# Optimization experiments

Measured on AMD Instinct MI355X. Metric: run time of the kernel, lower is better.

The kernel has to match this reference:

```python
import jax, jax.numpy as jnp
import numpy as np

N = 50000   # nodes
F = 128     # v_feats
K = 128     # filters
H = 3       # multi_head
M = 10      # fixed neighbor count (hardcoded repeat(1,10,1) in source)


def setup_inputs() -> dict:
    key = jax.random.key(0)
    ks = jax.random.split(key, 10)
    vertices = jax.random.normal(ks[0], (N, F), jnp.float32)
    nh_indices = jax.random.randint(ks[1], (N, M), 0, N)
    int_indices = jax.random.randint(ks[2], (N, M), 0, N)
    nh_edges = jax.random.uniform(ks[3], (N, M), jnp.float32)
    int_edges = jax.random.uniform(ks[4], (N, M), jnp.float32)
    is_int = jax.random.randint(ks[5], (N,), 0, 2)
    scale = 0.05
    Wvc = jax.random.normal(ks[6], (H, F, K), jnp.float32) * scale
    Wvn_int = jax.random.normal(ks[7], (H, F, K), jnp.float32) * scale
    Wvn_nh = jax.random.normal(ks[8], (H, F, K), jnp.float32) * scale
    a = jax.random.normal(ks[9], (H, 2 * K, 1), jnp.float32) * scale
    bv = jnp.zeros((H, K), jnp.float32)
    return dict(vertices=vertices, nh_indices=nh_indices, int_indices=int_indices,
                nh_edges=nh_edges, int_edges=int_edges, is_int=is_int,
                Wvc=Wvc, bv=bv, Wvn_int=Wvn_int, Wvn_nh=Wvn_nh, a=a)


def reference(vertices, nh_indices, int_indices, nh_edges, int_edges, is_int,
              Wvc, bv, Wvn_int, Wvn_nh, a):
    n = vertices.shape[0]
    k = a.shape[1] // 2
    # Project center and neighbor features for all heads at once.
    Zc = jnp.einsum('nf,hfk->hnk', vertices, Wvc)        # [H,N,K]
    Vint = jnp.einsum('nf,hfk->hnk', vertices, Wvn_int)  # [H,N,K]
    Vnh = jnp.einsum('nf,hfk->hnk', vertices, Wvn_nh)    # [H,N,K]
    # cat((neighbor, center)) @ a  ==  neighbor @ a[:k] + center @ a[k:]
    a_n = a[:, :k, 0]  # [H,K]
    a_c = a[:, k:, 0]  # [H,K]
    e_center = jnp.einsum('hnk,hk->hn', Zc, a_c)[:, :, None]  # [H,N,1]

    def branch(Vside, idx, edges):
        mask = (idx != -1).astype(vertices.dtype)           # [N,M], -1 = pad
        g = Vside[:, idx]                                   # [H,N,M,K] gather
        e = jnp.einsum('hnmk,hk->hnm', g, a_n) + e_center   # [H,N,M]
        # faithful to source: scores zeroed (not -inf) by mask/edges before softmax
        e = e * mask[None] * edges[None]
        alpha = jax.nn.softmax(e, axis=2)                   # [H,N,M]
        norm = jnp.maximum(mask.sum(axis=1), 1.0)           # [N]
        Zn = jnp.einsum('hnmk,hnm->hnk', g * mask[None, :, :, None], alpha)
        return Zn / norm[None, :, None]

    Zn_inter = branch(Vint, int_indices, int_edges)
    Zn_chain = branch(Vnh, nh_indices, nh_edges)
    z = jax.nn.relu(Zc + Zn_inter + Zn_chain + bv[:, None, :])  # [H,N,K]
    # torch.cat(head outputs, dim=1) -> [N, H*K]
    return jnp.transpose(z, (1, 0, 2)).reshape(n, -1)
```

## Files before the change

### kernel.cpp

```cpp
#include <hip/hip_runtime.h>
#include <stdint.h>

#define N_V 50000
#define F_DIM 128
#define K_DIM 128
#define H_DIM 3
#define M_DIM 10
#define TILES_PER_BLK 4

using bf16x8 = __attribute__((ext_vector_type(8))) short;
using f32x4  = __attribute__((ext_vector_type(4))) float;
using f32x2  = __attribute__((ext_vector_type(2))) float;
using h4     = __attribute__((ext_vector_type(4))) _Float16;

__device__ inline unsigned short f2bf(float f) {
    union { float f; uint32_t u; } v; v.f = f;
    uint32_t u = v.u;
    u += 0x7fffu + ((u >> 16) & 1u);
    return (unsigned short)(u >> 16);
}

__device__ inline uint32_t pkh2(float a, float b) {
    union { _Float16 h[2]; uint32_t u; } v;
    v.h[0] = (_Float16)a; v.h[1] = (_Float16)b;
    return v.u;
}

#define LDS_AS __attribute__((address_space(3)))
__device__ inline void gl2lds16(const void* g, void* l) {
    __builtin_amdgcn_global_load_lds(
        (const __attribute__((address_space(1))) unsigned int*)g,
        (LDS_AS unsigned int*)l, 16, 0, 0);
}

#define WTOT (9 * 128 * 128)
#define XCH  (N_V * 16)
#define WACT (9 * 128)

__global__ void prep(const float* __restrict__ Wvc,
                     const float* __restrict__ Wvn_int,
                     const float* __restrict__ Wvn_nh,
                     const float* __restrict__ X,
                     const float* __restrict__ a,
                     unsigned short* __restrict__ Wt,
                     unsigned short* __restrict__ Xb,
                     unsigned short* __restrict__ wab) {
    int idx = blockIdx.x * 256 + threadIdx.x;
    if (idx < WTOT) {
        int b   = idx >> 14;
        int rem = idx & 16383;
        int k = rem >> 7;
        int f = rem & 127;
        int h = b / 3, t = b - 3 * h;
        const float* src = (t == 0) ? Wvc : (t == 1) ? Wvn_int : Wvn_nh;
        Wt[idx] = f2bf(src[(h * 128 + f) * 128 + k]);
        return;
    }
    int xi = idx - WTOT;
    if (xi < XCH) {
        const float4* Xv = (const float4*)X;
        float4 v0 = Xv[xi * 2];
        float4 v1 = Xv[xi * 2 + 1];
        uint4 o;
        o.x = (uint32_t)f2bf(v0.x) | ((uint32_t)f2bf(v0.y) << 16);
        o.y = (uint32_t)f2bf(v0.z) | ((uint32_t)f2bf(v0.w) << 16);
        o.z = (uint32_t)f2bf(v1.x) | ((uint32_t)f2bf(v1.y) << 16);
        o.w = (uint32_t)f2bf(v1.z) | ((uint32_t)f2bf(v1.w) << 16);
        *(uint4*)&Xb[(size_t)xi * 8] = o;
        return;
    }
    int wi = xi - XCH;
    if (wi < WACT) {
        int b = wi >> 7, f = wi & 127;
        int h = b / 3, t = b - 3 * h;
        const float* src = (t == 0) ? Wvc : (t == 1) ? Wvn_int : Wvn_nh;
        const float4* wrow = (const float4*)&src[(h * 128 + f) * 128];
        const float4* av   = (const float4*)&a[h * 256 + (t == 0 ? 128 : 0)];
        float acc = 0.f;
        #pragma unroll 8
        for (int c = 0; c < 32; ++c) {
            float4 w = wrow[c], x = av[c];
            acc += w.x * x.x + w.y * x.y + w.z * x.z + w.w * x.w;
        }
        wab[b * 128 + f] = f2bf(acc);
    }
}

__global__ __launch_bounds__(256, 3) void gemm_kernel(
    const unsigned short* __restrict__ Xb,
    const unsigned short* __restrict__ Wt,
    const unsigned short* __restrict__ wab,
    _Float16* __restrict__ zc16,
    uint8_t* __restrict__ Vint,
    uint8_t* __restrict__ Vnh,
    float* __restrict__ ec4,
    float* __restrict__ ei4,
    float* __restrict__ en4) {
    __shared__ unsigned short As[2][64 * 128];

    const int tid  = threadIdx.x;
    const int b    = blockIdx.y;
    const int hh   = b / 3;
    const int tt   = b - 3 * hh;
    const int wv   = tid >> 6;
    const int lane = tid & 63;
    const int q    = lane >> 4;
    const int ln   = lane & 15;
    const int cb   = (wv >> 1) * 64;
    const int rb   = (wv & 1) * 32;
    const int m0   = blockIdx.x * (64 * TILES_PER_BLK);

    auto stage = [&](int buf, int tile) {
        const int mb = m0 + tile * 64;
        #pragma unroll
        for (int it = 0; it < 4; ++it) {
            int c16 = it * 256 + tid;
            int r   = c16 >> 4;
            int p   = c16 & 15;
            int lch = p ^ (r & 15);
            int gr  = mb + r;
            if (gr >= N_V) gr = 0;
            gl2lds16(Xb + (size_t)gr * 128 + lch * 8, &As[buf][c16 * 8]);
        }
    };

    stage(0, 0);

    const unsigned short* Wb = Wt + (size_t)b * 16384;
    bf16x8 bfr[4][4];
    #pragma unroll
    for (int ct = 0; ct < 4; ++ct) {
        int col = cb + 4 * ln + ct;
        #pragma unroll
        for (int kk = 0; kk < 4; ++kk)
            bfr[ct][kk] = *(const bf16x8*)&Wb[col * 128 + kk * 32 + q * 8];
    }

    const bool do_e = (b == 0) && (wv < 2);
    bf16x8 wz[4];
    if (do_e) {
        #pragma unroll
        for (int kk = 0; kk < 4; ++kk) {
            bf16x8 z = {0, 0, 0, 0, 0, 0, 0, 0};
            if (ln < 9) z = *(const bf16x8*)&wab[ln * 128 + kk * 32 + q * 8];
            wz[kk] = z;
        }
    }

    __syncthreads();

    const int c0 = cb + 4 * ln;
    #pragma unroll
    for (int t = 0; t < TILES_PER_BLK; ++t) {
        const int mb = m0 + t * 64;

        if (t + 1 < TILES_PER_BLK) stage((t + 1) & 1, t + 1);

        f32x4 acc[2][4];
        #pragma unroll
        for (int rt = 0; rt < 2; ++rt)
            #pragma unroll
            for (int ct = 0; ct < 4; ++ct) acc[rt][ct] = (f32x4){0.f, 0.f, 0.f, 0.f};

        #pragma unroll
        for (int rt = 0; rt < 2; ++rt) {
            bf16x8 afr[4];
            const int r = rb + rt * 16 + ln;
            #pragma unroll
            for (int kk = 0; kk < 4; ++kk) {
                int p = (kk * 4 + q) ^ ln;
                afr[kk] = *(const bf16x8*)&As[t & 1][r * 128 + p * 8];
            }
            #pragma unroll
            for (int kk = 0; kk < 4; ++kk)
                #pragma unroll
                for (int ct = 0; ct < 4; ++ct)
                    acc[rt][ct] = __builtin_amdgcn_mfma_f32_16x16x32_bf16(
                        afr[kk], bfr[ct][kk], acc[rt][ct], 0, 0, 0);

            if (do_e) {
                f32x4 ae = (f32x4){0.f, 0.f, 0.f, 0.f};
                #pragma unroll
                for (int kk = 0; kk < 4; ++kk)
                    ae = __builtin_amdgcn_mfma_f32_16x16x32_bf16(
                        afr[kk], wz[kk], ae, 0, 0, 0);
                if (ln < 9) {
                    int h2 = ln / 3, t2 = ln - 3 * h2;
                    float* ep = (t2 == 0) ? ec4 : (t2 == 1) ? ei4 : en4;
                    #pragma unroll
                    for (int rg = 0; rg < 4; ++rg) {
                        int gr = mb + rb + rt * 16 + q * 4 + rg;
                        if (gr < N_V) ep[gr * 4 + h2] = ae[rg];
                    }
                }
            }
        }

        __syncthreads();

        if (tt == 0) {
            #pragma unroll
            for (int rt = 0; rt < 2; ++rt)
                #pragma unroll
                for (int rg = 0; rg < 4; ++rg) {
                    int gr = mb + rb + rt * 16 + q * 4 + rg;
                    if (gr >= N_V) continue;
                    uint2 s;
                    s.x = pkh2(acc[rt][0][rg], acc[rt][1][rg]);
                    s.y = pkh2(acc[rt][2][rg], acc[rt][3][rg]);
                    *(uint2*)&zc16[(size_t)gr * 384 + hh * 128 + c0] = s;
                }
        } else {
            uint8_t* Vside = (tt == 1) ? Vint : Vnh;
            #pragma unroll
            for (int rt = 0; rt < 2; ++rt)
                #pragma unroll
                for (int rg = 0; rg < 4; ++rg) {
                    int gr = mb + rb + rt * 16 + q * 4 + rg;
                    if (gr >= N_V) continue;
                    int pk = __builtin_amdgcn_cvt_pk_fp8_f32(
                        acc[rt][0][rg], acc[rt][1][rg], 0, false);
                    pk = __builtin_amdgcn_cvt_pk_fp8_f32(
                        acc[rt][2][rg], acc[rt][3][rg], pk, true);
                    *(uint32_t*)&Vside[((size_t)gr * 3 + hh) * 128 + c0] =
                        (uint32_t)pk;
                }
        }
    }
}

__global__ __launch_bounds__(512) void attn_kernel(
    const int* __restrict__ nh_idx, const int* __restrict__ int_idx,
    const float* __restrict__ nh_edge, const float* __restrict__ int_edge,
    const float* __restrict__ bv,
    const uint8_t* __restrict__ Vint,
    const uint8_t* __restrict__ Vnh,
    const float* __restrict__ ec4, const float* __restrict__ ei4,
    const float* __restrict__ en4,
    const _Float16* __restrict__ zc16,
    float* __restrict__ out, int n0) {
    const int wv   = threadIdx.x >> 6;
    const int lane = threadIdx.x & 63;
    const int n    = n0 + blockIdx.x * 8 + wv;
    if (n >= N_V) return;
    const int g  = lane >> 4;
    const int gl = lane & 15;

    const bool part = (g <= 1) && (gl < M_DIM);
    int jm = -1; float wm = 0.f;
    if (part) {
        const int*   idx = (g == 0) ? int_idx  : nh_idx;
        const float* ed  = (g == 0) ? int_edge : nh_edge;
        jm = idx[n * M_DIM + gl];
        wm = ed[n * M_DIM + gl];
    }
    const bool  valid = part && (jm >= 0);
    const int   jc    = valid ? jm : 0;
    const float vfl   = valid ? 1.f : 0.f;

    const int src_base = (g < 2 ? 0 : 16) + (g & 1) * 5;
    int jrow[5];
    #pragma unroll
    for (int i = 0; i < 5; ++i) jrow[i] = __shfl(jc, src_base + i, 64);

    const uint8_t* Vb = (g < 2) ? Vint : Vnh;
    uint2 pv[3][5];
    #pragma unroll
    for (int i = 0; i < 5; ++i) {
        const uint8_t* base = Vb + (size_t)jrow[i] * 384 + gl * 8;
        #pragma unroll
        for (int h = 0; h < H_DIM; ++h)
            pv[h][i] = *(const uint2*)(base + h * 128);
    }
    float4 ev = make_float4(0.f, 0.f, 0.f, 0.f);
    if (part) ev = *(const float4*)&(((g == 0) ? ei4 : en4)[jc * 4]);
    const float4 ecv = *(const float4*)&ec4[n * 4];

    float4 zc[3], bb[3];
    if (g < 2) {
        #pragma unroll
        for (int h = 0; h < H_DIM; ++h) {
            h4 z = *(const h4*)&zc16[(size_t)n * 384 + h * 128 + gl * 8 + g * 4];
            zc[h] = make_float4((float)z[0], (float)z[1], (float)z[2], (float)z[3]);
            bb[h] = *(const float4*)&bv[h * 128 + gl * 8 + g * 4];
        }
    }

    float cf = vfl;
    #pragma unroll
    for (int off = 1; off < 16; off <<= 1) cf += __shfl_xor(cf, off, 64);
    const float cnorm = fmaxf(cf, 1.f);

    #pragma unroll
    for (int h = 0; h < H_DIM; ++h) {
        const float eh  = (h == 0) ? ev.x  : (h == 1) ? ev.y  : ev.z;
        const float ech = (h == 0) ? ecv.x : (h == 1) ? ecv.y : ecv.z;

        float l = (part && valid) ? (eh + ech) * wm : 0.f;
        float ex = part ? __expf(l) : 0.f;
        float sv = ex;
        #pragma unroll
        for (int off = 1; off < 16; off <<= 1) sv += __shfl_xor(sv, off, 64);
        float alphap = valid ? ex / (sv * cnorm) : 0.f;

        f32x2 acc2[4];
        #pragma unroll
        for (int c = 0; c < 4; ++c) acc2[c] = (f32x2){0.f, 0.f};
        #pragma unroll
        for (int i = 0; i < 5; ++i) {
            float al = __shfl(alphap, src_base + i, 64);
            f32x2 al2 = (f32x2){al, al};
            uint2 p  = pv[h][i];
            f32x2 f01 = __builtin_amdgcn_cvt_pk_f32_fp8(p.x, false);
            f32x2 f23 = __builtin_amdgcn_cvt_pk_f32_fp8(p.x, true);
            f32x2 f45 = __builtin_amdgcn_cvt_pk_f32_fp8(p.y, false);
            f32x2 f67 = __builtin_amdgcn_cvt_pk_f32_fp8(p.y, true);
            acc2[0] += al2 * f01;
            acc2[1] += al2 * f23;
            acc2[2] += al2 * f45;
            acc2[3] += al2 * f67;
        }
        #pragma unroll
        for (int c = 0; c < 4; ++c) {
            f32x2 v = acc2[c];
            v.x += __shfl_xor(v.x, 16, 64);
            v.y += __shfl_xor(v.y, 16, 64);
            v.x += __shfl_xor(v.x, 32, 64);
            v.y += __shfl_xor(v.y, 32, 64);
            acc2[c] = v;
        }
        if (g < 2) {
            size_t o = (size_t)n * 384 + h * 128 + gl * 8 + g * 4;
            float4 zn;
            if (g == 0) zn = make_float4(acc2[0].x, acc2[0].y, acc2[1].x, acc2[1].y);
            else        zn = make_float4(acc2[2].x, acc2[2].y, acc2[3].x, acc2[3].y);
            float4 r;
            r.x = fmaxf(zc[h].x + zn.x + bb[h].x, 0.f);
            r.y = fmaxf(zc[h].y + zn.y + bb[h].y, 0.f);
            r.z = fmaxf(zc[h].z + zn.z + bb[h].z, 0.f);
            r.w = fmaxf(zc[h].w + zn.w + bb[h].w, 0.f);
            *(float4*)&out[o] = r;
        }
    }
}

extern "C" void kernel_launch(void* const* d_in, const int* in_sizes, int n_in,
                              void* d_out, int out_size, void* d_ws, size_t ws_size,
                              hipStream_t stream) {
    const float* vertices    = (const float*)d_in[0];
    const int*   nh_indices  = (const int*)d_in[1];
    const int*   int_indices = (const int*)d_in[2];
    const float* nh_edges    = (const float*)d_in[3];
    const float* int_edges   = (const float*)d_in[4];
    const float* Wvc     = (const float*)d_in[6];
    const float* bv      = (const float*)d_in[7];
    const float* Wvn_int = (const float*)d_in[8];
    const float* Wvn_nh  = (const float*)d_in[9];
    const float* a       = (const float*)d_in[10];
    float* out = (float*)d_out;

    char* ws = (char*)d_ws;
    size_t off = 0;
    unsigned short* Wt = (unsigned short*)(ws + off);
    off += (size_t)WTOT * 2;                  off = (off + 255) & ~(size_t)255;
    unsigned short* wab = (unsigned short*)(ws + off);
    off += (size_t)WACT * 2;                  off = (off + 255) & ~(size_t)255;
    unsigned short* Xb = (unsigned short*)(ws + off);
    off += (size_t)N_V * 128 * 2;             off = (off + 255) & ~(size_t)255;
    uint8_t* Vint = (uint8_t*)(ws + off);
    off += (size_t)H_DIM * N_V * 128;         off = (off + 255) & ~(size_t)255;
    uint8_t* Vnh = (uint8_t*)(ws + off);
    off += (size_t)H_DIM * N_V * 128;         off = (off + 255) & ~(size_t)255;
    _Float16* zc16 = (_Float16*)(ws + off);
    off += (size_t)N_V * 384 * 2;             off = (off + 255) & ~(size_t)255;
    float* ec4 = (float*)(ws + off);
    off += (size_t)N_V * 4 * 4;               off = (off + 255) & ~(size_t)255;
    float* ei4 = (float*)(ws + off);
    off += (size_t)N_V * 4 * 4;               off = (off + 255) & ~(size_t)255;
    float* en4 = (float*)(ws + off);
    off += (size_t)N_V * 4 * 4;

    int prep_threads = WTOT + XCH + WACT;
    prep<<<(prep_threads + 255) / 256, 256, 0, stream>>>(
        Wvc, Wvn_int, Wvn_nh, vertices, a, Wt, Xb, wab);

    dim3 grid_g((N_V + 64 * TILES_PER_BLK - 1) / (64 * TILES_PER_BLK), 9);
    gemm_kernel<<<grid_g, 256, 0, stream>>>(Xb, Wt, wab, zc16, Vint, Vnh,
                                            ec4, ei4, en4);

    attn_kernel<<<3125, 512, 0, stream>>>(
        nh_indices, int_indices, nh_edges, int_edges, bv,
        Vint, Vnh, ec4, ei4, en4, zc16, out, 0);
    attn_kernel<<<3125, 512, 0, stream>>>(
        nh_indices, int_indices, nh_edges, int_edges, bv,
        Vint, Vnh, ec4, ei4, en4, zc16, out, 25000);
}
```

Before: 235.3 us.

## Alias center projection into output buffer, remap GEMM blocks per XCD, merge attention launches

The fp16 center projection is now written into the first half of each output row instead of a separate workspace buffer. The attention kernel reads it back from the same row before overwriting that row with fp32 results. The GEMM grid is flattened and remapped so that consecutive row tiles and head/type combinations land on the same XCD, aiming for better L2 reuse of the input tiles. The two half-size attention launches become one launch with 256-thread blocks and an occupancy hint, and empty asm statements force all gathered loads to be issued before compute. The in-place aliasing depends on each wave reading its whole row before writing it, which adds a subtle correctness dependency.

Result: faster. 222.1 us, median of 2 (-5.6%).

```diff
diff --git a/kernel.cpp b/kernel.cpp
--- a/kernel.cpp
+++ b/kernel.cpp
@@ -7,6 +7,9 @@
 #define H_DIM 3
 #define M_DIM 10
 #define TILES_PER_BLK 4
+#define NBLK 1764
+#define BLK_PER_XCD 221
+#define NBLK_PAD 1768
 
 using bf16x8 = __attribute__((ext_vector_type(8))) short;
 using f32x4  = __attribute__((ext_vector_type(4))) float;
@@ -98,17 +101,23 @@
     float* __restrict__ en4) {
     __shared__ unsigned short As[2][64 * 128];
 
+    const int xc = blockIdx.x & 7;
+    const int sq = blockIdx.x >> 3;
+    const int gB = xc * BLK_PER_XCD + sq;
+    if (gB >= NBLK) return;
+    const int x  = gB / 9;
+    const int b  = gB - 9 * x;
+    const int hh = b / 3;
+    const int tt = b - 3 * hh;
+
     const int tid  = threadIdx.x;
-    const int b    = blockIdx.y;
-    const int hh   = b / 3;
-    const int tt   = b - 3 * hh;
     const int wv   = tid >> 6;
     const int lane = tid & 63;
     const int q    = lane >> 4;
     const int ln   = lane & 15;
     const int cb   = (wv >> 1) * 64;
     const int rb   = (wv & 1) * 32;
-    const int m0   = blockIdx.x * (64 * TILES_PER_BLK);
+    const int m0   = x * (64 * TILES_PER_BLK);
 
     auto stage = [&](int buf, int tile) {
         const int mb = m0 + tile * 64;
@@ -208,7 +217,7 @@
                     uint2 s;
                     s.x = pkh2(acc[rt][0][rg], acc[rt][1][rg]);
                     s.y = pkh2(acc[rt][2][rg], acc[rt][3][rg]);
-                    *(uint2*)&zc16[(size_t)gr * 384 + hh * 128 + c0] = s;
+                    *(uint2*)&zc16[(size_t)gr * 768 + hh * 128 + c0] = s;
                 }
         } else {
             uint8_t* Vside = (tt == 1) ? Vint : Vnh;
@@ -229,7 +238,7 @@
     }
 }
 
-__global__ __launch_bounds__(512) void attn_kernel(
+__global__ __launch_bounds__(256, 4) void attn_kernel(
     const int* __restrict__ nh_idx, const int* __restrict__ int_idx,
     const float* __restrict__ nh_edge, const float* __restrict__ int_edge,
     const float* __restrict__ bv,
@@ -237,14 +246,15 @@
     const uint8_t* __restrict__ Vnh,
     const float* __restrict__ ec4, const float* __restrict__ ei4,
     const float* __restrict__ en4,
-    const _Float16* __restrict__ zc16,
-    float* __restrict__ out, int n0) {
+    float* __restrict__ out) {
+    const _Float16* zcp = (const _Float16*)out;
     const int wv   = threadIdx.x >> 6;
     const int lane = threadIdx.x & 63;
-    const int n    = n0 + blockIdx.x * 8 + wv;
+    const int n    = blockIdx.x * 4 + wv;
     if (n >= N_V) return;
     const int g  = lane >> 4;
     const int gl = lane & 15;
+    const int gg = g & 1;
 
     const bool part = (g <= 1) && (gl < M_DIM);
     int jm = -1; float wm = 0.f;
@@ -277,19 +287,30 @@
     const float4 ecv = *(const float4*)&ec4[n * 4];
 
     float4 zc[3], bb[3];
-    if (g < 2) {
-        #pragma unroll
-        for (int h = 0; h < H_DIM; ++h) {
-            h4 z = *(const h4*)&zc16[(size_t)n * 384 + h * 128 + gl * 8 + g * 4];
-            zc[h] = make_float4((float)z[0], (float)z[1], (float)z[2], (float)z[3]);
-            bb[h] = *(const float4*)&bv[h * 128 + gl * 8 + g * 4];
-        }
+    #pragma unroll
+    for (int h = 0; h < H_DIM; ++h) {
+        h4 z = *(const h4*)&zcp[(size_t)n * 768 + h * 128 + gl * 8 + gg * 4];
+        zc[h] = make_float4((float)z[0], (float)z[1], (float)z[2], (float)z[3]);
+        bb[h] = *(const float4*)&bv[h * 128 + gl * 8 + gg * 4];
     }
 
     float cf = vfl;
     #pragma unroll
     for (int off = 1; off < 16; off <<= 1) cf += __shfl_xor(cf, off, 64);
     const float cnorm = fmaxf(cf, 1.f);
+
+    #pragma unroll
+    for (int h = 0; h < H_DIM; ++h)
+        #pragma unroll
+        for (int i = 0; i < 5; ++i)
+            asm volatile("" :: "v"(pv[h][i].x), "v"(pv[h][i].y));
+    asm volatile("" :: "v"(ev.x), "v"(ev.y), "v"(ev.z));
+    asm volatile("" :: "v"(ecv.x), "v"(ecv.y), "v"(ecv.z));
+    #pragma unroll
+    for (int h = 0; h < H_DIM; ++h) {
+        asm volatile("" :: "v"(zc[h].x), "v"(zc[h].y), "v"(zc[h].z), "v"(zc[h].w));
+        asm volatile("" :: "v"(bb[h].x), "v"(bb[h].y), "v"(bb[h].z), "v"(bb[h].w));
+    }
 
     #pragma unroll
     for (int h = 0; h < H_DIM; ++h) {
@@ -371,8 +392,6 @@
     off += (size_t)H_DIM * N_V * 128;         off = (off + 255) & ~(size_t)255;
     uint8_t* Vnh = (uint8_t*)(ws + off);
     off += (size_t)H_DIM * N_V * 128;         off = (off + 255) & ~(size_t)255;
-    _Float16* zc16 = (_Float16*)(ws + off);
-    off += (size_t)N_V * 384 * 2;             off = (off + 255) & ~(size_t)255;
     float* ec4 = (float*)(ws + off);
     off += (size_t)N_V * 4 * 4;               off = (off + 255) & ~(size_t)255;
     float* ei4 = (float*)(ws + off);
@@ -384,14 +403,10 @@
     prep<<<(prep_threads + 255) / 256, 256, 0, stream>>>(
         Wvc, Wvn_int, Wvn_nh, vertices, a, Wt, Xb, wab);
 
-    dim3 grid_g((N_V + 64 * TILES_PER_BLK - 1) / (64 * TILES_PER_BLK), 9);
-    gemm_kernel<<<grid_g, 256, 0, stream>>>(Xb, Wt, wab, zc16, Vint, Vnh,
-                                            ec4, ei4, en4);
-
-    attn_kernel<<<3125, 512, 0, stream>>>(
+    gemm_kernel<<<NBLK_PAD, 256, 0, stream>>>(
+        Xb, Wt, wab, (_Float16*)out, Vint, Vnh, ec4, ei4, en4);
+
+    attn_kernel<<<(N_V + 3) / 4, 256, 0, stream>>>(
         nh_indices, int_indices, nh_edges, int_edges, bv,
-        Vint, Vnh, ec4, ei4, en4, zc16, out, 0);
-    attn_kernel<<<3125, 512, 0, stream>>>(
-        nh_indices, int_indices, nh_edges, int_edges, bv,
-        Vint, Vnh, ec4, ei4, en4, zc16, out, 25000);
-}
+        Vint, Vnh, ec4, ei4, en4, out);
+}
```
